# Optimization experiments

Hardware: AMD Instinct MI355X
Metric: run time of the kernel (lower is better)

## Reference

```python
import jax, jax.numpy as jnp
import numpy as np

SIGMA = 0.07        # kernel width param; gamma = 1/sigma
K_NEG = 16          # hard negatives per anchor
BS = 8192
DIM = 256

def setup_inputs() -> dict:
    key = jax.random.key(0)
    features = jax.random.normal(key, (BS, 2, DIM), dtype=jnp.float32)
    return {"features": features}

def reference(features):
    gamma = 1.0 / float(SIGMA)
    F1 = features[:, 0, :].astype(jnp.float32)   # (bs, d)
    F2 = features[:, 1, :].astype(jnp.float32)   # (bs, d)
    # RBF-style kernel: exp(-gamma * (2 - 2 * F1 @ F2^T))
    K = jnp.exp(-gamma * (2.0 - 2.0 * jnp.einsum('id,jd->ij', F1, F2)))  # (bs, bs)
    pos_loss = jnp.mean(jnp.diagonal(K))
    # mask diagonal with -inf, take row-wise top-k, mean over all selected
    eye = jnp.eye(BS, dtype=bool)
    neg = jnp.where(eye, -jnp.inf, K)
    topk_vals, _ = jax.lax.top_k(neg, K_NEG)     # (bs, k)
    hard_neg_loss = jnp.mean(topk_vals)
    return (-pos_loss, hard_neg_loss)
```

## Files before the change

kernel.cpp:

```cpp
#include <hip/hip_runtime.h>
#include <math.h>

#define BS   8192
#define DIM  256
#define KNEG 16
#define GAMMA (1.0f / 0.07f)
#define EXP_CLAMP 60.0f
#define NSTRIPS 8

typedef float v4f  __attribute__((ext_vector_type(4)));
typedef short s8b  __attribute__((ext_vector_type(8)));

__device__ __forceinline__ float sat_exp(float dot) {
    float a = 2.0f * GAMMA * dot - 2.0f * GAMMA;
    return expf(fminf(a, EXP_CLAMP));
}

__device__ __forceinline__ void ce(float& x, float& y) {
    float lo = fminf(x, y), hi = fmaxf(x, y);
    x = lo; y = hi;
}

__device__ __forceinline__ void sort16(float (&a)[16]) {
    ce(a[0],a[1]); ce(a[2],a[3]); ce(a[4],a[5]); ce(a[6],a[7]);
    ce(a[8],a[9]); ce(a[10],a[11]); ce(a[12],a[13]); ce(a[14],a[15]);
    ce(a[0],a[2]); ce(a[1],a[3]); ce(a[4],a[6]); ce(a[5],a[7]);
    ce(a[8],a[10]); ce(a[9],a[11]); ce(a[12],a[14]); ce(a[13],a[15]);
    ce(a[1],a[2]); ce(a[5],a[6]); ce(a[9],a[10]); ce(a[13],a[14]);
    ce(a[0],a[4]); ce(a[1],a[5]); ce(a[2],a[6]); ce(a[3],a[7]);
    ce(a[8],a[12]); ce(a[9],a[13]); ce(a[10],a[14]); ce(a[11],a[15]);
    ce(a[2],a[4]); ce(a[3],a[5]); ce(a[10],a[12]); ce(a[11],a[13]);
    ce(a[1],a[2]); ce(a[3],a[4]); ce(a[5],a[6]);
    ce(a[9],a[10]); ce(a[11],a[12]); ce(a[13],a[14]);
    ce(a[0],a[8]); ce(a[1],a[9]); ce(a[2],a[10]); ce(a[3],a[11]);
    ce(a[4],a[12]); ce(a[5],a[13]); ce(a[6],a[14]); ce(a[7],a[15]);
    ce(a[4],a[8]); ce(a[5],a[9]); ce(a[6],a[10]); ce(a[7],a[11]);
    ce(a[2],a[4]); ce(a[3],a[5]); ce(a[6],a[8]); ce(a[7],a[9]);
    ce(a[10],a[12]); ce(a[11],a[13]);
    ce(a[1],a[2]); ce(a[3],a[4]); ce(a[5],a[6]); ce(a[7],a[8]);
    ce(a[9],a[10]); ce(a[11],a[12]); ce(a[13],a[14]);
}

__device__ __forceinline__ void merge_top16(float (&lst)[16], const float (&nw)[16]) {
#pragma unroll
    for (int i = 0; i < 16; ++i) lst[i] = fmaxf(lst[i], nw[15 - i]);
#pragma unroll
    for (int j = 8; j > 0; j >>= 1)
#pragma unroll
        for (int i = 0; i < 16; ++i) {
            int ixj = i ^ j;
            if (ixj > i) ce(lst[i], lst[ixj]);
        }
}

__device__ __forceinline__ void topk_insert(float (&lst)[16], float v) {
    float nl[16];
#pragma unroll
    for (int u = 0; u < 15; ++u)
        nl[u] = (v > lst[u + 1]) ? lst[u + 1] : ((v > lst[u]) ? v : lst[u]);
    nl[15] = (v > lst[15]) ? v : lst[15];
#pragma unroll
    for (int u = 0; u < 16; ++u) lst[u] = nl[u];
}

__device__ __forceinline__ unsigned short f2bf_rne(float f) {
    unsigned int u = __float_as_uint(f);
    u += 0x7FFFu + ((u >> 16) & 1u);
    return (unsigned short)(u >> 16);
}

__device__ __forceinline__ void gld_lds16(const void* g, void* l) {
    __builtin_amdgcn_global_load_lds(
        (const __attribute__((address_space(1))) void*)g,
        (__attribute__((address_space(3))) void*)l, 16, 0, 0);
}

__device__ __forceinline__ float finite_or(float x, float repl) {
    if (isnan(x)) return repl;
    if (isinf(x)) return x > 0.0f ? 3.0e38f : -3.0e38f;
    return x;
}

__global__ void conv_pos(const float* __restrict__ feat,
                         unsigned short* __restrict__ featbf,
                         float* __restrict__ partialPos) {
    __shared__ float red[8];
    int t = blockIdx.x * 256 + threadIdx.x;
    int row = t >> 5;
    int c = t & 31;
    const float* f1 = feat + (size_t)row * 512 + c * 8;
    const float* f2 = f1 + 256;
    float4 a0 = *(const float4*)(f1);
    float4 a1 = *(const float4*)(f1 + 4);
    float4 b0 = *(const float4*)(f2);
    float4 b1 = *(const float4*)(f2 + 4);
    uint4 pa, pb;
    pa.x = (unsigned)f2bf_rne(a0.x) | ((unsigned)f2bf_rne(a0.y) << 16);
    pa.y = (unsigned)f2bf_rne(a0.z) | ((unsigned)f2bf_rne(a0.w) << 16);
    pa.z = (unsigned)f2bf_rne(a1.x) | ((unsigned)f2bf_rne(a1.y) << 16);
    pa.w = (unsigned)f2bf_rne(a1.z) | ((unsigned)f2bf_rne(a1.w) << 16);
    pb.x = (unsigned)f2bf_rne(b0.x) | ((unsigned)f2bf_rne(b0.y) << 16);
    pb.y = (unsigned)f2bf_rne(b0.z) | ((unsigned)f2bf_rne(b0.w) << 16);
    pb.z = (unsigned)f2bf_rne(b1.x) | ((unsigned)f2bf_rne(b1.y) << 16);
    pb.w = (unsigned)f2bf_rne(b1.z) | ((unsigned)f2bf_rne(b1.w) << 16);
    *(uint4*)(featbf + (size_t)row * 512 + c * 8) = pa;
    *(uint4*)(featbf + (size_t)row * 512 + 256 + c * 8) = pb;
    float p = a0.x * b0.x + a0.y * b0.y + a0.z * b0.z + a0.w * b0.w
            + a1.x * b1.x + a1.y * b1.y + a1.z * b1.z + a1.w * b1.w;
#pragma unroll
    for (int o = 16; o; o >>= 1) p += __shfl_xor(p, o, 32);
    if (c == 0) red[threadIdx.x >> 5] = sat_exp(p);
    __syncthreads();
    if (threadIdx.x == 0) {
        float s = 0.0f;
#pragma unroll
        for (int i = 0; i < 8; ++i) s += red[i];
        partialPos[blockIdx.x] = s;
    }
}

#define A_OFF  32768
#define S1_LDS 49152

__global__ __launch_bounds__(256, 3) void stage1(const unsigned short* __restrict__ featbf,
                                                 float* __restrict__ wsTop) {
    __shared__ __align__(16) char smem[S1_LDS];
    const int t = threadIdx.x;
    const int l = t & 63;
    const int w = t >> 6;
    const int wy = w >> 1, wx = w & 1;
    const int quad = l >> 4, lane16 = l & 15;
    const int nbase = blockIdx.x * 64;
    const int strip = blockIdx.y;
    const bool dstrip = (strip == (nbase >> 10));
    const int dct = (nbase & 1023) >> 7;

#pragma unroll
    for (int jj = 0; jj < 8; ++jj) {
        int j = w * 8 + jj;
        int r = 2 * j + (l >> 5);
        int c = (l & 31) ^ (r & 31);
        gld_lds16(featbf + ((size_t)(nbase + r) << 9) + c * 8, smem + j * 1024);
    }

    float lst[2][16];
#pragma unroll
    for (int ni = 0; ni < 2; ++ni)
#pragma unroll
        for (int i = 0; i < 16; ++i) lst[ni][i] = -INFINITY;

    const int akey = (quad ^ ((lane16 >> 1) & 3)) * 16;
    const int sj_r = l >> 2;
    const int sj_s = l & 3;

    {
        const int ctbase = strip * 1024;
#pragma unroll
        for (int jj = 0; jj < 2; ++jj) {
            int j = w * 2 + jj;
            int r = 16 * j + sj_r;
            int c = sj_s ^ ((r >> 1) & 3);
            gld_lds16(featbf + ((size_t)(ctbase + r) << 9) + 256 + c * 8,
                      smem + A_OFF + j * 1024);
        }
    }

#pragma unroll 1
    for (int ct = 0; ct < 8; ++ct) {
        const int ctbase = strip * 1024 + ct * 128;
        v4f acc[4][2];
#pragma unroll
        for (int mi = 0; mi < 4; ++mi)
#pragma unroll
            for (int ni = 0; ni < 2; ++ni) acc[mi][ni] = (v4f)0.0f;

#pragma unroll
        for (int s = 0; s < 8; ++s) {
            __syncthreads();
            if (ct < 7 || s < 7) {
                const int nct = (s == 7) ? ctbase + 128 : ctbase;
                const int ns = (s == 7) ? 0 : s + 1;
                char* dst = smem + A_OFF + ((s + 1) & 1) * 8192;
#pragma unroll
                for (int jj = 0; jj < 2; ++jj) {
                    int j = w * 2 + jj;
                    int r = 16 * j + sj_r;
                    int c = sj_s ^ ((r >> 1) & 3);
                    gld_lds16(featbf + ((size_t)(nct + r) << 9) + 256 + ns * 32 + c * 8,
                              dst + j * 1024);
                }
            }
            const char* Ab = smem + A_OFF + (s & 1) * 8192;
            s8b a[4];
#pragma unroll
            for (int mi = 0; mi < 4; ++mi)
                a[mi] = *(const s8b*)(Ab + (wx * 64 + mi * 16 + lane16) * 64 + akey);
#pragma unroll
            for (int ni = 0; ni < 2; ++ni) {
                int n31 = ni * 16 + lane16;
                s8b b = *(const s8b*)(smem
                    + (wy * 32 + n31) * 512 + (((s * 4 + quad) ^ n31) & 31) * 16);
#pragma unroll
                for (int mi = 0; mi < 4; ++mi)
                    acc[mi][ni] = __builtin_amdgcn_mfma_f32_16x16x32_bf16(
                        a[mi], b, acc[mi][ni], 0, 0, 0);
            }
        }
        const bool dohere = dstrip && (ct == dct);
#pragma unroll
        for (int ni = 0; ni < 2; ++ni) {
            float nw[16];
#pragma unroll
            for (int mi = 0; mi < 4; ++mi)
#pragma unroll
                for (int r4 = 0; r4 < 4; ++r4)
                    nw[mi * 4 + r4] = acc[mi][ni][r4];
            if (dohere) {
                const int row = nbase + wy * 32 + ni * 16 + lane16;
#pragma unroll
                for (int mi = 0; mi < 4; ++mi) {
                    const int c0 = ctbase + wx * 64 + mi * 16 + quad * 4;
#pragma unroll
                    for (int r4 = 0; r4 < 4; ++r4)
                        if (c0 + r4 == row) nw[mi * 4 + r4] = -INFINITY;
                }
            }
            sort16(nw);
            merge_top16(lst[ni], nw);
        }
    }
#pragma unroll
    for (int ni = 0; ni < 2; ++ni) {
#pragma unroll
        for (int r = 16; r <= 32; r <<= 1) {
            float nw[16];
#pragma unroll
            for (int i = 0; i < 16; ++i) nw[i] = __shfl(lst[ni][i], l ^ r, 64);
            merge_top16(lst[ni], nw);
        }
    }
    __syncthreads();
    float* mrg = (float*)(smem + A_OFF);
    if (wx == 1 && quad == 0) {
#pragma unroll
        for (int ni = 0; ni < 2; ++ni) {
            int rl = wy * 32 + ni * 16 + lane16;
#pragma unroll
            for (int i = 0; i < 16; i += 4)
                *(v4f*)(mrg + rl * 16 + i) = *(v4f*)&lst[ni][i];
        }
    }
    __syncthreads();
    if (wx == 0 && quad == 0) {
#pragma unroll
        for (int ni = 0; ni < 2; ++ni) {
            const int rl = wy * 32 + ni * 16 + lane16;
            float nw[16];
#pragma unroll
            for (int i = 0; i < 16; ++i) nw[i] = mrg[rl * 16 + i];
            merge_top16(lst[ni], nw);
            float* dst = wsTop + ((size_t)(nbase + rl) * NSTRIPS + strip) * 16;
#pragma unroll
            for (int i = 0; i < 16; i += 4)
                *(float4*)(dst + i) = make_float4(lst[ni][i], lst[ni][i + 1],
                                                  lst[ni][i + 2], lst[ni][i + 3]);
        }
    }
}

__global__ void stage2_fast(const float* __restrict__ wsTop, float* __restrict__ partialNeg) {
    __shared__ float red[128];
    int tid = blockIdx.x * 128 + threadIdx.x;
    int row = tid >> 1, half = tid & 1;
    const float* src = wsTop + (size_t)row * (NSTRIPS * 16) + half * 64;
    float lst[16];
#pragma unroll
    for (int i = 0; i < 16; ++i) lst[i] = src[i];
#pragma unroll
    for (int c = 16; c < 64; c += 16) {
        float nw[16];
#pragma unroll
        for (int i = 0; i < 16; ++i) nw[i] = src[c + i];
        merge_top16(lst, nw);
    }
    {
        float nw[16];
        int pl = (threadIdx.x & 63) ^ 1;
#pragma unroll
        for (int i = 0; i < 16; ++i) nw[i] = __shfl(lst[i], pl, 64);
        merge_top16(lst, nw);
    }
    float s = 0.0f;
#pragma unroll
    for (int i = 0; i < 16; ++i) s += sat_exp(lst[i]);
    red[threadIdx.x] = half ? 0.0f : s;
    __syncthreads();
    for (int o = 64; o; o >>= 1) {
        if (threadIdx.x < o) red[threadIdx.x] += red[threadIdx.x + o];
        __syncthreads();
    }
    if (threadIdx.x == 0) partialNeg[blockIdx.x] = red[0];
}

__global__ void final_kernel(const float* __restrict__ partialPos,
                             const float* __restrict__ partialNeg,
                             float* __restrict__ out) {
    __shared__ float w1[4], w2[4];
    float sp = 0.0f, sn = 0.0f;
    for (int i = threadIdx.x; i < 1024; i += 256) sp += partialPos[i];
    if (threadIdx.x < 128) sn = partialNeg[threadIdx.x];
#pragma unroll
    for (int o = 32; o; o >>= 1) {
        sp += __shfl_xor(sp, o, 64);
        sn += __shfl_xor(sn, o, 64);
    }
    if ((threadIdx.x & 63) == 0) {
        w1[threadIdx.x >> 6] = sp;
        w2[threadIdx.x >> 6] = sn;
    }
    __syncthreads();
    if (threadIdx.x == 0) {
        float tp = w1[0] + w1[1] + w1[2] + w1[3];
        float tn = w2[0] + w2[1] + w2[2] + w2[3];
        out[0] = finite_or(-(tp / (float)BS), 0.0f);
        out[1] = finite_or(tn / (float)(BS * KNEG), 0.0f);
    }
}

__global__ void init_acc(float* acc) {
    if (threadIdx.x < 64) acc[threadIdx.x] = 0.0f;
}

__global__ void pos_kernel(const float* __restrict__ feat, float* __restrict__ acc) {
    int t = blockIdx.x * 256 + threadIdx.x;
    int row = t >> 4;
    int lane16 = t & 15;
    const float* f = feat + (size_t)row * 512 + lane16 * 16;
    float p = 0.0f;
#pragma unroll
    for (int q = 0; q < 16; q += 4) {
        float4 a = *(const float4*)(f + q);
        float4 b = *(const float4*)(f + 256 + q);
        p += a.x * b.x + a.y * b.y + a.z * b.z + a.w * b.w;
    }
#pragma unroll
    for (int o = 8; o; o >>= 1) p += __shfl_xor(p, o, 16);
    if (lane16 == 0) atomicAdd(&acc[0], sat_exp(p));
}

#define L_AOFF   0
#define L_BOFF   10240
#define L_PITCH  80
#define CPITCH  272
#define CWAVE   17408
#define L_SMEM  69632
__global__ __launch_bounds__(256, 2) void stage1_legacy(const float* __restrict__ feat,
                                                        float* __restrict__ wsTop) {
    __shared__ __align__(16) char smem[L_SMEM];
    const int t = threadIdx.x;
    const int l = t & 63;
    const int w = t >> 6;
    const int wy = w >> 1, wx = w & 1;
    const int quad = l >> 4, lane16 = l & 15;
    const int rowbase = blockIdx.x * 128;
    const int strip = blockIdx.y;
    char* cw = smem + w * CWAVE;
    const int grow = rowbase + wy * 64 + l;

    float lst[16];
#pragma unroll
    for (int i = 0; i < 16; ++i) lst[i] = -INFINITY;

    for (int ct = 0; ct < 4; ++ct) {
        const int colbase = strip * 1024 + ct * 256;
        v4f acc[4][8];
#pragma unroll
        for (int mi = 0; mi < 4; ++mi)
#pragma unroll
            for (int ni = 0; ni < 8; ++ni) acc[mi][ni] = (v4f)0.0f;
        for (int s = 0; s < 8; ++s) {
            const int k0 = s * 32;
            __syncthreads();
#pragma unroll
            for (int i = 0; i < 4; ++i) {
                int c = i * 256 + t;
                int r = c >> 3, chk = c & 7;
                float4 v = *(const float4*)(feat + (size_t)(rowbase + r) * 512 + k0 + chk * 4);
                uint2 pk;
                pk.x = (unsigned)f2bf_rne(v.x) | ((unsigned)f2bf_rne(v.y) << 16);
                pk.y = (unsigned)f2bf_rne(v.z) | ((unsigned)f2bf_rne(v.w) << 16);
                *(uint2*)(smem + L_AOFF + r * L_PITCH + chk * 8) = pk;
            }
#pragma unroll
            for (int i = 0; i < 8; ++i) {
                int c = i * 256 + t;
                int n = c >> 3, chk = c & 7;
                float4 v = *(const float4*)(feat + (size_t)(colbase + n) * 512 + 256 + k0 + chk * 4);
                uint2 pk;
                pk.x = (unsigned)f2bf_rne(v.x) | ((unsigned)f2bf_rne(v.y) << 16);
                pk.y = (unsigned)f2bf_rne(v.z) | ((unsigned)f2bf_rne(v.w) << 16);
                *(uint2*)(smem + L_BOFF + n * L_PITCH + chk * 8) = pk;
            }
            __syncthreads();
            s8b a[4];
#pragma unroll
            for (int mi = 0; mi < 4; ++mi)
                a[mi] = *(const s8b*)(smem + L_AOFF + (wy * 64 + mi * 16 + lane16) * L_PITCH + quad * 16);
#pragma unroll
            for (int ni = 0; ni < 8; ++ni) {
                s8b b = *(const s8b*)(smem + L_BOFF + (wx * 128 + ni * 16 + lane16) * L_PITCH + quad * 16);
#pragma unroll
                for (int mi = 0; mi < 4; ++mi)
                    acc[mi][ni] = __builtin_amdgcn_mfma_f32_16x16x32_bf16(a[mi], b, acc[mi][ni], 0, 0, 0);
            }
        }
#pragma unroll
        for (int h = 0; h < 2; ++h) {
            __syncthreads();
#pragma unroll
            for (int ni = 0; ni < 4; ++ni) {
                int c = ni * 16 + lane16;
#pragma unroll
                for (int mi = 0; mi < 4; ++mi)
                    *(v4f*)(cw + c * CPITCH + mi * 64 + quad * 16) = acc[mi][h * 4 + ni];
            }
            __syncthreads();
            const int gc0 = colbase + wx * 128 + h * 64;
            const int dj = grow - gc0;
#pragma unroll
            for (int j = 0; j < 64; ++j) {
                float v = *(const float*)(cw + j * CPITCH + l * 4);
                if (v > lst[0] && j != dj) topk_insert(lst, v);
            }
        }
    }
    float* dst = wsTop + (size_t)grow * 256 + strip * 32 + wx * 16;
#pragma unroll
    for (int i = 0; i < 16; i += 4)
        *(float4*)(dst + i) = make_float4(lst[i], lst[i + 1], lst[i + 2], lst[i + 3]);
}

__global__ void stage2_legacy(const float* __restrict__ wsTop, float* __restrict__ acc) {
    int row = blockIdx.x * blockDim.x + threadIdx.x;
    if (row >= BS) return;
    const float* src = wsTop + (size_t)row * 256;
    float lst[16];
#pragma unroll
    for (int i = 0; i < 16; ++i) lst[i] = -INFINITY;
    for (int c = 0; c < 256; c += 4) {
        float4 v4 = *(const float4*)(src + c);
        float vv[4] = {v4.x, v4.y, v4.z, v4.w};
#pragma unroll
        for (int j = 0; j < 4; ++j)
            if (vv[j] > lst[0]) topk_insert(lst, vv[j]);
    }
    float s = 0.0f;
#pragma unroll
    for (int i = 0; i < 16; ++i) s += sat_exp(lst[i]);
    atomicAdd(&acc[1], s);
}

__global__ void final_legacy(const float* __restrict__ acc, float* __restrict__ out) {
    if (threadIdx.x == 0) {
        out[0] = finite_or(-(acc[0] / (float)BS), 0.0f);
        out[1] = finite_or(acc[1] / (float)(BS * KNEG), 0.0f);
    }
}

extern "C" void kernel_launch(void* const* d_in, const int* in_sizes, int n_in,
                              void* d_out, int out_size, void* d_ws, size_t ws_size,
                              hipStream_t stream) {
    const float* feat = (const float*)d_in[0];
    float* out = (float*)d_out;

    unsigned short* featbf = (unsigned short*)d_ws;
    float* wsTop = (float*)(featbf + (size_t)BS * 512);
    float* partialPos = wsTop + (size_t)BS * NSTRIPS * 16;
    float* partialNeg = partialPos + 1024;
    const size_t need_new = (size_t)BS * 512 * 2 + (size_t)BS * NSTRIPS * 16 * 4
                          + (1024 + 128) * 4;

    if (ws_size >= need_new) {
        conv_pos<<<1024, 256, 0, stream>>>(feat, featbf, partialPos);
        stage1<<<dim3(128, NSTRIPS), 256, 0, stream>>>(featbf, wsTop);
        stage2_fast<<<128, 128, 0, stream>>>(wsTop, partialNeg);
        final_kernel<<<1, 256, 0, stream>>>(partialPos, partialNeg, out);
    } else {
        float* acc = (float*)d_ws;
        float* wsTopL = acc + 64;
        init_acc<<<1, 64, 0, stream>>>(acc);
        pos_kernel<<<512, 256, 0, stream>>>(feat, acc);
        stage1_legacy<<<dim3(64, 8), 256, 0, stream>>>(feat, wsTopL);
        stage2_legacy<<<32, 256, 0, stream>>>(wsTopL, acc);
        final_legacy<<<1, 1, 0, stream>>>(acc, out);
    }
}
```

Baseline: 135.4 us.

## Pack two rows' top-k sorting into fp16x2 and keep B fragments in registers

The per-tile top-16 selection now runs on packed half2 values, so one sort and merge network serves two rows at once instead of running separate float networks per row. This cuts the compare/exchange VALU work roughly in half. The B-operand fragments for the block's rows are also loaded from LDS once into registers, rather than re-read in every k-step of every column tile. In exchange, candidate dot products are rounded to fp16 with round-toward-zero before selection, which loses precision and range, and the cached fragments add 64 VGPRs of pressure that may lower occupancy.

```diff
diff --git a/kernel.cpp b/kernel.cpp
--- a/kernel.cpp
+++ b/kernel.cpp
@@ -10,35 +10,59 @@
 
 typedef float v4f  __attribute__((ext_vector_type(4)));
 typedef short s8b  __attribute__((ext_vector_type(8)));
+typedef _Float16 h2 __attribute__((ext_vector_type(2)));
 
 __device__ __forceinline__ float sat_exp(float dot) {
     float a = 2.0f * GAMMA * dot - 2.0f * GAMMA;
     return expf(fminf(a, EXP_CLAMP));
 }
 
+__device__ __forceinline__ h2 pk2(float a, float b) {
+    return __builtin_bit_cast(h2, __builtin_amdgcn_cvt_pkrtz(a, b));
+}
+
 __device__ __forceinline__ void ce(float& x, float& y) {
     float lo = fminf(x, y), hi = fmaxf(x, y);
     x = lo; y = hi;
 }
 
-__device__ __forceinline__ void sort16(float (&a)[16]) {
-    ce(a[0],a[1]); ce(a[2],a[3]); ce(a[4],a[5]); ce(a[6],a[7]);
-    ce(a[8],a[9]); ce(a[10],a[11]); ce(a[12],a[13]); ce(a[14],a[15]);
-    ce(a[0],a[2]); ce(a[1],a[3]); ce(a[4],a[6]); ce(a[5],a[7]);
-    ce(a[8],a[10]); ce(a[9],a[11]); ce(a[12],a[14]); ce(a[13],a[15]);
-    ce(a[1],a[2]); ce(a[5],a[6]); ce(a[9],a[10]); ce(a[13],a[14]);
-    ce(a[0],a[4]); ce(a[1],a[5]); ce(a[2],a[6]); ce(a[3],a[7]);
-    ce(a[8],a[12]); ce(a[9],a[13]); ce(a[10],a[14]); ce(a[11],a[15]);
-    ce(a[2],a[4]); ce(a[3],a[5]); ce(a[10],a[12]); ce(a[11],a[13]);
-    ce(a[1],a[2]); ce(a[3],a[4]); ce(a[5],a[6]);
-    ce(a[9],a[10]); ce(a[11],a[12]); ce(a[13],a[14]);
-    ce(a[0],a[8]); ce(a[1],a[9]); ce(a[2],a[10]); ce(a[3],a[11]);
-    ce(a[4],a[12]); ce(a[5],a[13]); ce(a[6],a[14]); ce(a[7],a[15]);
-    ce(a[4],a[8]); ce(a[5],a[9]); ce(a[6],a[10]); ce(a[7],a[11]);
-    ce(a[2],a[4]); ce(a[3],a[5]); ce(a[6],a[8]); ce(a[7],a[9]);
-    ce(a[10],a[12]); ce(a[11],a[13]);
-    ce(a[1],a[2]); ce(a[3],a[4]); ce(a[5],a[6]); ce(a[7],a[8]);
-    ce(a[9],a[10]); ce(a[11],a[12]); ce(a[13],a[14]);
+__device__ __forceinline__ void ce2(h2& x, h2& y) {
+    h2 lo = __builtin_elementwise_min(x, y);
+    h2 hi = __builtin_elementwise_max(x, y);
+    x = lo; y = hi;
+}
+
+__device__ __forceinline__ void sort16p(h2 (&a)[16]) {
+    ce2(a[0],a[1]); ce2(a[2],a[3]); ce2(a[4],a[5]); ce2(a[6],a[7]);
+    ce2(a[8],a[9]); ce2(a[10],a[11]); ce2(a[12],a[13]); ce2(a[14],a[15]);
+    ce2(a[0],a[2]); ce2(a[1],a[3]); ce2(a[4],a[6]); ce2(a[5],a[7]);
+    ce2(a[8],a[10]); ce2(a[9],a[11]); ce2(a[12],a[14]); ce2(a[13],a[15]);
+    ce2(a[1],a[2]); ce2(a[5],a[6]); ce2(a[9],a[10]); ce2(a[13],a[14]);
+    ce2(a[0],a[4]); ce2(a[1],a[5]); ce2(a[2],a[6]); ce2(a[3],a[7]);
+    ce2(a[8],a[12]); ce2(a[9],a[13]); ce2(a[10],a[14]); ce2(a[11],a[15]);
+    ce2(a[2],a[4]); ce2(a[3],a[5]); ce2(a[10],a[12]); ce2(a[11],a[13]);
+    ce2(a[1],a[2]); ce2(a[3],a[4]); ce2(a[5],a[6]);
+    ce2(a[9],a[10]); ce2(a[11],a[12]); ce2(a[13],a[14]);
+    ce2(a[0],a[8]); ce2(a[1],a[9]); ce2(a[2],a[10]); ce2(a[3],a[11]);
+    ce2(a[4],a[12]); ce2(a[5],a[13]); ce2(a[6],a[14]); ce2(a[7],a[15]);
+    ce2(a[4],a[8]); ce2(a[5],a[9]); ce2(a[6],a[10]); ce2(a[7],a[11]);
+    ce2(a[2],a[4]); ce2(a[3],a[5]); ce2(a[6],a[8]); ce2(a[7],a[9]);
+    ce2(a[10],a[12]); ce2(a[11],a[13]);
+    ce2(a[1],a[2]); ce2(a[3],a[4]); ce2(a[5],a[6]); ce2(a[7],a[8]);
+    ce2(a[9],a[10]); ce2(a[11],a[12]); ce2(a[13],a[14]);
+}
+
+__device__ __forceinline__ void merge2_top16(h2 (&lst)[16], const h2 (&nw)[16]) {
+#pragma unroll
+    for (int i = 0; i < 16; ++i)
+        lst[i] = __builtin_elementwise_max(lst[i], nw[15 - i]);
+#pragma unroll
+    for (int j = 8; j > 0; j >>= 1)
+#pragma unroll
+        for (int i = 0; i < 16; ++i) {
+            int ixj = i ^ j;
+            if (ixj > i) ce2(lst[i], lst[ixj]);
+        }
 }
 
 __device__ __forceinline__ void merge_top16(float (&lst)[16], const float (&nw)[16]) {
@@ -79,6 +103,12 @@
     if (isnan(x)) return repl;
     if (isinf(x)) return x > 0.0f ? 3.0e38f : -3.0e38f;
     return x;
+}
+
+__device__ __forceinline__ h2 shfl2(h2 x, int src) {
+    float f = __builtin_bit_cast(float, x);
+    f = __shfl(f, src, 64);
+    return __builtin_bit_cast(h2, f);
 }
 
 __global__ void conv_pos(const float* __restrict__ feat,
@@ -143,11 +173,10 @@
         gld_lds16(featbf + ((size_t)(nbase + r) << 9) + c * 8, smem + j * 1024);
     }
 
-    float lst[2][16];
-#pragma unroll
-    for (int ni = 0; ni < 2; ++ni)
-#pragma unroll
-        for (int i = 0; i < 16; ++i) lst[ni][i] = -INFINITY;
+    h2 lst[16];
+    const h2 NINF = __builtin_bit_cast(h2, 0xFC00FC00u);
+#pragma unroll
+    for (int i = 0; i < 16; ++i) lst[i] = NINF;
 
     const int akey = (quad ^ ((lane16 >> 1) & 3)) * 16;
     const int sj_r = l >> 2;
@@ -163,6 +192,17 @@
             gld_lds16(featbf + ((size_t)(ctbase + r) << 9) + 256 + c * 8,
                       smem + A_OFF + j * 1024);
         }
+    }
+
+    __syncthreads();
+    s8b bfr[16];
+#pragma unroll
+    for (int ni = 0; ni < 2; ++ni) {
+        const int n31 = ni * 16 + lane16;
+#pragma unroll
+        for (int s = 0; s < 8; ++s)
+            bfr[ni * 8 + s] = *(const s8b*)(smem
+                + (wy * 32 + n31) * 512 + (((s * 4 + quad) ^ n31) & 31) * 16);
     }
 
 #pragma unroll 1
@@ -196,74 +236,67 @@
             for (int mi = 0; mi < 4; ++mi)
                 a[mi] = *(const s8b*)(Ab + (wx * 64 + mi * 16 + lane16) * 64 + akey);
 #pragma unroll
-            for (int ni = 0; ni < 2; ++ni) {
-                int n31 = ni * 16 + lane16;
-                s8b b = *(const s8b*)(smem
-                    + (wy * 32 + n31) * 512 + (((s * 4 + quad) ^ n31) & 31) * 16);
+            for (int ni = 0; ni < 2; ++ni)
 #pragma unroll
                 for (int mi = 0; mi < 4; ++mi)
                     acc[mi][ni] = __builtin_amdgcn_mfma_f32_16x16x32_bf16(
-                        a[mi], b, acc[mi][ni], 0, 0, 0);
-            }
+                        a[mi], bfr[ni * 8 + s], acc[mi][ni], 0, 0, 0);
         }
         const bool dohere = dstrip && (ct == dct);
-#pragma unroll
-        for (int ni = 0; ni < 2; ++ni) {
-            float nw[16];
+        h2 nw[16];
+        if (dohere) {
+            const int row0 = nbase + wy * 32 + lane16;
+#pragma unroll
+            for (int mi = 0; mi < 4; ++mi) {
+                const int c0 = ctbase + wx * 64 + mi * 16 + quad * 4;
+#pragma unroll
+                for (int r4 = 0; r4 < 4; ++r4) {
+                    float v0 = acc[mi][0][r4];
+                    float v1 = acc[mi][1][r4];
+                    if (c0 + r4 == row0) v0 = -INFINITY;
+                    if (c0 + r4 == row0 + 16) v1 = -INFINITY;
+                    nw[mi * 4 + r4] = pk2(v0, v1);
+                }
+            }
+        } else {
 #pragma unroll
             for (int mi = 0; mi < 4; ++mi)
 #pragma unroll
                 for (int r4 = 0; r4 < 4; ++r4)
-                    nw[mi * 4 + r4] = acc[mi][ni][r4];
-            if (dohere) {
-                const int row = nbase + wy * 32 + ni * 16 + lane16;
-#pragma unroll
-                for (int mi = 0; mi < 4; ++mi) {
-                    const int c0 = ctbase + wx * 64 + mi * 16 + quad * 4;
-#pragma unroll
-                    for (int r4 = 0; r4 < 4; ++r4)
-                        if (c0 + r4 == row) nw[mi * 4 + r4] = -INFINITY;
-                }
-            }
-            sort16(nw);
-            merge_top16(lst[ni], nw);
-        }
-    }
-#pragma unroll
-    for (int ni = 0; ni < 2; ++ni) {
-#pragma unroll
-        for (int r = 16; r <= 32; r <<= 1) {
-            float nw[16];
-#pragma unroll
-            for (int i = 0; i < 16; ++i) nw[i] = __shfl(lst[ni][i], l ^ r, 64);
-            merge_top16(lst[ni], nw);
-        }
+                    nw[mi * 4 + r4] = pk2(acc[mi][0][r4], acc[mi][1][r4]);
+        }
+        sort16p(nw);
+        merge2_top16(lst, nw);
+    }
+#pragma unroll
+    for (int r = 16; r <= 32; r <<= 1) {
+        h2 nw[16];
+#pragma unroll
+        for (int i = 0; i < 16; ++i) nw[i] = shfl2(lst[i], l ^ r);
+        merge2_top16(lst, nw);
     }
     __syncthreads();
-    float* mrg = (float*)(smem + A_OFF);
+    h2* mrg = (h2*)(smem + A_OFF);
     if (wx == 1 && quad == 0) {
-#pragma unroll
-        for (int ni = 0; ni < 2; ++ni) {
-            int rl = wy * 32 + ni * 16 + lane16;
-#pragma unroll
-            for (int i = 0; i < 16; i += 4)
-                *(v4f*)(mrg + rl * 16 + i) = *(v4f*)&lst[ni][i];
-        }
+        const int rl = wy * 16 + lane16;
+#pragma unroll
+        for (int i = 0; i < 16; ++i) mrg[rl * 16 + i] = lst[i];
     }
     __syncthreads();
     if (wx == 0 && quad == 0) {
+        const int rl = wy * 16 + lane16;
+        h2 nw[16];
+#pragma unroll
+        for (int i = 0; i < 16; ++i) nw[i] = mrg[rl * 16 + i];
+        merge2_top16(lst, nw);
 #pragma unroll
         for (int ni = 0; ni < 2; ++ni) {
-            const int rl = wy * 32 + ni * 16 + lane16;
-            float nw[16];
-#pragma unroll
-            for (int i = 0; i < 16; ++i) nw[i] = mrg[rl * 16 + i];
-            merge_top16(lst[ni], nw);
-            float* dst = wsTop + ((size_t)(nbase + rl) * NSTRIPS + strip) * 16;
+            const int grow = nbase + wy * 32 + ni * 16 + lane16;
+            float* dst = wsTop + ((size_t)grow * NSTRIPS + strip) * 16;
 #pragma unroll
             for (int i = 0; i < 16; i += 4)
-                *(float4*)(dst + i) = make_float4(lst[ni][i], lst[ni][i + 1],
-                                                  lst[ni][i + 2], lst[ni][i + 3]);
+                *(float4*)(dst + i) = make_float4((float)lst[i][ni], (float)lst[i + 1][ni],
+                                                  (float)lst[i + 2][ni], (float)lst[i + 3][ni]);
         }
     }
 }
```

Measured after the change: 124.7 us. 7.9% less time.
